# Kernel tuning notes

Measured on AMD Instinct MI355X. Metric: run time of the kernel, lower is better.

The kernel has to match this reference:

```python
import jax, jax.numpy as jnp
import numpy as np

N_NODES = 50000
N_EDGES = 800000
D = 128
BN_EPS = 1e-5


def setup_inputs() -> dict:
    key = jax.random.key(0)
    k1, k2, k3, k4 = jax.random.split(key, 4)
    feature = jax.random.normal(k1, (N_NODES, D), dtype=jnp.float32)
    W = jax.random.normal(k2, (D, D), dtype=jnp.float32) * (1.0 / np.sqrt(D))
    b = jnp.zeros((D,), dtype=jnp.float32)
    gamma = jnp.ones((D,), dtype=jnp.float32)
    beta = jnp.zeros((D,), dtype=jnp.float32)
    src = jax.random.randint(k3, (N_EDGES,), 0, N_NODES, dtype=jnp.int64)
    dst = jax.random.randint(k4, (N_EDGES,), 0, N_NODES, dtype=jnp.int64)
    return {"feature": feature, "W": W, "b": b, "gamma": gamma, "beta": beta,
            "src": src, "dst": dst}


def reference(feature, W, b, gamma, beta, src, dst):
    # --- message passing: copy_u + mean over in-neighbors ---
    n = feature.shape[0]
    msgs = feature[src]  # [E, D] gather of source node features
    agg = jax.ops.segment_sum(msgs, dst, num_segments=n)  # [N, D]
    deg = jax.ops.segment_sum(jnp.ones((src.shape[0],), feature.dtype), dst,
                              num_segments=n)  # [N]
    h = jnp.where(deg[:, None] > 0, agg / jnp.maximum(deg, 1.0)[:, None], 0.0)
    # --- node apply: linear ---
    h = h @ W.T + b
    # --- BatchNorm1d (training mode: biased batch stats over node dim) ---
    mu = jnp.mean(h, axis=0)
    var = jnp.mean(jnp.square(h - mu), axis=0)
    h = (h - mu) / jnp.sqrt(var + BN_EPS) * gamma + beta
    # --- activation + residual (dropout p=0 is identity) ---
    h = jax.nn.relu(h)
    h = feature + h
    return h
```

## Files before the change

kernel.cpp:

```cpp
#include <hip/hip_runtime.h>
#include <cstddef>
#include <cstdint>

#define N_NODES 50000
#define N_EDGES 800000
#define D 128
#define BN_EPS 1e-5f

#define NBUCKET 782
#define BCAP 1536
#define PART_BLOCKS 256
#define PART_CHUNK 3125
#define SLOTS 48
#define SLOTS_P 50
#define GEMM_CHUNKS 1563
#define GEMM_GRID   512
#define FEAT_V8     (N_NODES * D / 8)
#define SLICE_V8    (N_NODES * 4)
#define W_V8        (D * D / 8)
#define CAST_BLOCKS ((FEAT_V8 + W_V8 + 255) / 256)
#define ZERO_V4     3192

typedef __attribute__((ext_vector_type(8))) short short8_t;
typedef __attribute__((ext_vector_type(8))) unsigned short u16x8;
typedef __attribute__((ext_vector_type(4))) float f32x4;
typedef __attribute__((ext_vector_type(4))) int i32x4;

#define WS_STAT_OFF    0
#define WS_GCUR_OFF    1024
#define WS_WB_OFF      51072
#define WS_CLAIM_OFF   83840
#define WS_HB_OFF      4888448
#define WS_H2_OFF      17688448
#define WS_FB_OFF      30488448

static __device__ __forceinline__ unsigned short f2bf(float x) {
    unsigned u = __float_as_uint(x);
    unsigned r = (u + 0x7fffu + ((u >> 16) & 1u)) >> 16;
    return (unsigned short)r;
}
static __device__ __forceinline__ float bf2f(unsigned short v) {
    return __uint_as_float(((unsigned)v) << 16);
}

__global__ __launch_bounds__(256) void prezero_k(i32x4* __restrict__ zws) {
    int i = blockIdx.x * 256 + threadIdx.x;
    if (i < ZERO_V4) zws[i] = (i32x4){0, 0, 0, 0};
}

__global__ __launch_bounds__(256) void castpart_k(const float* __restrict__ feat,
                                                  const float* __restrict__ W,
                                                  u16x8* __restrict__ fb,
                                                  u16x8* __restrict__ wb,
                                                  const int* __restrict__ src,
                                                  const int* __restrict__ dst,
                                                  int* __restrict__ gcur,
                                                  unsigned* __restrict__ claims) {
    __shared__ unsigned pk[PART_CHUNK];
    __shared__ int hist[NBUCKET];
    __shared__ int base_l[NBUCKET];
    const int t = threadIdx.x;

    if (blockIdx.x < PART_BLOCKS) {
        const int base = blockIdx.x * PART_CHUNK;

        for (int b = t; b < NBUCKET; b += 256) hist[b] = 0;
        __syncthreads();

        for (int i = t; i < PART_CHUNK; i += 256) {
            int s = src[base + i];
            int d = dst[base + i];
            pk[i] = ((unsigned)s << 16) | (unsigned)d;
            atomicAdd(&hist[d >> 6], 1);
        }
        __syncthreads();

        for (int b = t; b < NBUCKET; b += 256) {
            int h = hist[b];
            base_l[b] = h ? atomicAdd(gcur + b * 16, h) : 0;
            hist[b] = 0;
        }
        __syncthreads();

        for (int i = t; i < PART_CHUNK; i += 256) {
            unsigned u = pk[i];
            int bkt = (int)(u & 0xffffu) >> 6;
            int k = atomicAdd(&hist[bkt], 1);
            int pos = base_l[bkt] + k;
            if (pos < BCAP) claims[bkt * BCAP + pos] = u;
        }
    } else {
        int i = (blockIdx.x - PART_BLOCKS) * 256 + t;
        if (i < FEAT_V8) {
            int q  = i / SLICE_V8;
            int r  = i - q * SLICE_V8;
            int n  = r >> 2, oc = r & 3;
            const f32x4* fp = reinterpret_cast<const f32x4*>(feat + n * D + q * 32 + oc * 8);
            f32x4 x0 = __builtin_nontemporal_load(fp);
            f32x4 x1 = __builtin_nontemporal_load(fp + 1);
            u16x8 o;
            o[0] = f2bf(x0.x); o[1] = f2bf(x0.y); o[2] = f2bf(x0.z); o[3] = f2bf(x0.w);
            o[4] = f2bf(x1.x); o[5] = f2bf(x1.y); o[6] = f2bf(x1.z); o[7] = f2bf(x1.w);
            __builtin_nontemporal_store(o, fb + i);
        } else if (i < FEAT_V8 + W_V8) {
            int j = i - FEAT_V8;
            const f32x4* fp = reinterpret_cast<const f32x4*>(W) + j * 2;
            f32x4 x0 = __builtin_nontemporal_load(fp);
            f32x4 x1 = __builtin_nontemporal_load(fp + 1);
            u16x8 o;
            o[0] = f2bf(x0.x); o[1] = f2bf(x0.y); o[2] = f2bf(x0.z); o[3] = f2bf(x0.w);
            o[4] = f2bf(x1.x); o[5] = f2bf(x1.y); o[6] = f2bf(x1.z); o[7] = f2bf(x1.w);
            __builtin_nontemporal_store(o, wb + j);
        }
    }
}

__global__ __launch_bounds__(256) void bingather_k(const int* __restrict__ gcur,
                                                   const unsigned* __restrict__ claims,
                                                   const u16x8* __restrict__ fb,
                                                   u16x8* __restrict__ hb) {
    __shared__ unsigned short ebl[64 * SLOTS_P];
    __shared__ int lcnt[64];
    const int t = threadIdx.x;
    const int b = blockIdx.x >> 2;
    const int q = blockIdx.x & 3;
    const u16x8* fbq = fb + (size_t)q * SLICE_V8;

    if (t < 64) lcnt[t] = 0;
    __syncthreads();

    const int n = min(gcur[b * 16], BCAP);
    const unsigned* cp = claims + b * BCAP;
    for (int i = t; i < n; i += 256) {
        unsigned u = cp[i];
        int dl = (int)(u & 63u);
        int k = atomicAdd(&lcnt[dl], 1);
        if (k < SLOTS) ebl[dl * SLOTS_P + k] = (unsigned short)(u >> 16);
    }
    __syncthreads();

    const int nl = t >> 2;
    const int oc = t & 3;
    const int node = (b << 6) + nl;
    const int deg = lcnt[nl];
    const int nd  = min(deg, SLOTS);
    const unsigned short* slots = ebl + nl * SLOTS_P;

    float a[8];
#pragma unroll
    for (int i = 0; i < 8; ++i) a[i] = 0.f;

    int e = 0;
    for (; e + 4 <= nd; e += 4) {
        int s0 = slots[e],     s1 = slots[e + 1];
        int s2 = slots[e + 2], s3 = slots[e + 3];
        u16x8 v0 = fbq[s0 * 4 + oc];
        u16x8 v1 = fbq[s1 * 4 + oc];
        u16x8 v2 = fbq[s2 * 4 + oc];
        u16x8 v3 = fbq[s3 * 4 + oc];
#pragma unroll
        for (int i = 0; i < 8; ++i) a[i] += (bf2f(v0[i]) + bf2f(v1[i])) +
                                            (bf2f(v2[i]) + bf2f(v3[i]));
    }
    for (; e < nd; ++e) {
        u16x8 v0 = fbq[(int)slots[e] * 4 + oc];
#pragma unroll
        for (int i = 0; i < 8; ++i) a[i] += bf2f(v0[i]);
    }

    if (node < N_NODES) {
        float inv = (deg > 0) ? 1.f / (float)deg : 0.f;
        u16x8 o;
#pragma unroll
        for (int i = 0; i < 8; ++i) o[i] = f2bf(a[i] * inv);
        hb[(size_t)q * SLICE_V8 + node * 4 + oc] = o;
    }
}

__global__ __launch_bounds__(256) void gemm_mfma_k(const u16x8* __restrict__ hb,
                                                   const u16x8* __restrict__ wb,
                                                   const float* __restrict__ bias,
                                                   unsigned short* __restrict__ h2,
                                                   float* __restrict__ colsum,
                                                   float* __restrict__ colsumsq) {
    const int wave = threadIdx.x >> 6;
    const int lane = threadIdx.x & 63;
    const int wm = wave >> 1, wn = wave & 1;
    const int l15 = lane & 15, l4 = lane >> 4;

    short8_t bf[4][4];
#pragma unroll
    for (int t = 0; t < 4; ++t) {
        const int col = wn * 64 + t * 16 + l15;
#pragma unroll
        for (int s = 0; s < 4; ++s) {
            u16x8 w = wb[col * 16 + s * 4 + l4];
            short8_t b8;
#pragma unroll
            for (int i = 0; i < 8; ++i) b8[i] = (short)w[i];
            bf[t][s] = b8;
        }
    }
    float bc[4];
#pragma unroll
    for (int t = 0; t < 4; ++t) bc[t] = bias[wn * 64 + t * 16 + l15];

    float s1[4] = {0.f, 0.f, 0.f, 0.f};
    float s2[4] = {0.f, 0.f, 0.f, 0.f};

    for (int chunk = blockIdx.x; chunk < GEMM_CHUNKS; chunk += gridDim.x) {
        const int rbase = chunk * 32 + wm * 16;
        const int arow = min(rbase + l15, N_NODES - 1);
        short8_t af[4];
#pragma unroll
        for (int s = 0; s < 4; ++s) {
            u16x8 hv8 = hb[(size_t)s * SLICE_V8 + arow * 4 + l4];
            short8_t t8;
#pragma unroll
            for (int i = 0; i < 8; ++i) t8[i] = (short)hv8[i];
            af[s] = t8;
        }

        f32x4 acc[4];
#pragma unroll
        for (int t = 0; t < 4; ++t) acc[t] = (f32x4){0.f, 0.f, 0.f, 0.f};

#pragma unroll
        for (int s = 0; s < 4; ++s)
#pragma unroll
            for (int t = 0; t < 4; ++t)
                acc[t] = __builtin_amdgcn_mfma_f32_16x16x32_bf16(af[s], bf[t][s],
                                                                 acc[t], 0, 0, 0);

        const int orow0 = rbase + l4 * 4;
#pragma unroll
        for (int t = 0; t < 4; ++t) {
            const int col = wn * 64 + t * 16 + l15;
#pragma unroll
            for (int r = 0; r < 4; ++r) {
                const int row = orow0 + r;
                if (row < N_NODES) {
                    float hv = acc[t][r] + bc[t];
                    h2[(size_t)row * D + col] = f2bf(hv);
                    s1[t] += hv;
                    s2[t] += hv * hv;
                }
            }
        }
    }

#pragma unroll
    for (int t = 0; t < 4; ++t) {
        s1[t] += __shfl_xor(s1[t], 16); s1[t] += __shfl_xor(s1[t], 32);
        s2[t] += __shfl_xor(s2[t], 16); s2[t] += __shfl_xor(s2[t], 32);
    }
    if (lane < 16) {
#pragma unroll
        for (int t = 0; t < 4; ++t) {
            int col = wn * 64 + t * 16 + lane;
            atomicAdd(colsum + col, s1[t]);
            atomicAdd(colsumsq + col, s2[t]);
        }
    }
}

__global__ __launch_bounds__(256) void epilogue_k(const u16x8* __restrict__ h2v,
                                                  const float* __restrict__ feat,
                                                  const float* __restrict__ colsum,
                                                  const float* __restrict__ colsumsq,
                                                  const float* __restrict__ gamma,
                                                  const float* __restrict__ beta,
                                                  float* __restrict__ out) {
    int idx = blockIdx.x * 256 + threadIdx.x;
    if (idx >= FEAT_V8) return;
    const int colb = (idx * 8) & 127;
    const float inv_n = 1.0f / N_NODES;

    u16x8 hv8 = h2v[idx];
    const float4* fp = reinterpret_cast<const float4*>(feat) + idx * 2;
    float4 fv0 = fp[0], fv1 = fp[1];
    float4 o0, o1;
#pragma unroll
    for (int i = 0; i < 8; ++i) {
        int c = colb + i;
        float mu  = colsum[c] * inv_n;
        float var = colsumsq[c] * inv_n - mu * mu;
        float a   = gamma[c] * rsqrtf(var + BN_EPS);
        float bb  = beta[c] - mu * a;
        float hv  = bf2f(hv8[i]);
        float fv  = (i < 4) ? (&fv0.x)[i] : (&fv1.x)[i - 4];
        float ov  = fv + fmaxf(hv * a + bb, 0.f);
        if (i < 4) (&o0.x)[i] = ov; else (&o1.x)[i - 4] = ov;
    }
    float4* op = reinterpret_cast<float4*>(out) + idx * 2;
    op[0] = o0;
    op[1] = o1;
}

extern "C" void kernel_launch(void* const* d_in, const int* in_sizes, int n_in,
                              void* d_out, int out_size, void* d_ws, size_t ws_size,
                              hipStream_t stream) {
    const float* feature = (const float*)d_in[0];
    const float* W       = (const float*)d_in[1];
    const float* b       = (const float*)d_in[2];
    const float* gamma   = (const float*)d_in[3];
    const float* beta    = (const float*)d_in[4];
    const int*   src     = (const int*)d_in[5];
    const int*   dst     = (const int*)d_in[6];
    float* out = (float*)d_out;

    char* ws = (char*)d_ws;
    float*          colsum   = (float*)(ws + WS_STAT_OFF);
    float*          colsumsq = colsum + 128;
    int*            gcur     = (int*)(ws + WS_GCUR_OFF);
    u16x8*          wb       = (u16x8*)(ws + WS_WB_OFF);
    unsigned*       claims   = (unsigned*)(ws + WS_CLAIM_OFF);
    u16x8*          hb       = (u16x8*)(ws + WS_HB_OFF);
    unsigned short* h2       = (unsigned short*)(ws + WS_H2_OFF);
    u16x8*          fb       = (u16x8*)(ws + WS_FB_OFF);

    prezero_k<<<13, 256, 0, stream>>>((i32x4*)ws);
    castpart_k<<<PART_BLOCKS + CAST_BLOCKS, 256, 0, stream>>>(
        feature, W, fb, wb, src, dst, gcur, claims);
    bingather_k<<<NBUCKET * 4, 256, 0, stream>>>(gcur, claims, fb, hb);
    gemm_mfma_k<<<GEMM_GRID, 256, 0, stream>>>(hb, wb, b, h2, colsum, colsumsq);
    epilogue_k<<<(FEAT_V8 + 255) / 256, 256, 0, stream>>>(
        (u16x8*)h2, feature, colsum, colsumsq, gamma, beta, out);
}
```

Baseline: 105.3 us.

## Fuse GEMM and BatchNorm epilogue into one cooperative kernel with grid sync

The GEMM kernel and the BatchNorm/ReLU/residual epilogue kernel become a single cooperative launch, with a grid-wide barrier after the column-statistics atomics. Each thread computes its per-column scale and shift once, then loops over row chunks writing the output. This removes one kernel launch and the per-element recomputation of the column statistics. It adds grid-sync overhead and requires all 512 blocks to be co-resident. The src/dst index loads also switch to nontemporal loads.

```diff
diff --git a/kernel.cpp b/kernel.cpp
--- a/kernel.cpp
+++ b/kernel.cpp
@@ -1,6 +1,9 @@
 #include <hip/hip_runtime.h>
+#include <hip/hip_cooperative_groups.h>
 #include <cstddef>
 #include <cstdint>
+
+namespace cg = cooperative_groups;
 
 #define N_NODES 50000
 #define N_EDGES 800000
@@ -68,8 +71,8 @@
         __syncthreads();
 
         for (int i = t; i < PART_CHUNK; i += 256) {
-            int s = src[base + i];
-            int d = dst[base + i];
+            int s = __builtin_nontemporal_load(src + base + i);
+            int d = __builtin_nontemporal_load(dst + base + i);
             pk[i] = ((unsigned)s << 16) | (unsigned)d;
             atomicAdd(&hist[d >> 6], 1);
         }
@@ -177,12 +180,16 @@
     }
 }
 
-__global__ __launch_bounds__(256) void gemm_mfma_k(const u16x8* __restrict__ hb,
-                                                   const u16x8* __restrict__ wb,
-                                                   const float* __restrict__ bias,
-                                                   unsigned short* __restrict__ h2,
-                                                   float* __restrict__ colsum,
-                                                   float* __restrict__ colsumsq) {
+__global__ __launch_bounds__(256) void gemmepi_k(const u16x8* __restrict__ hb,
+                                                 const u16x8* __restrict__ wb,
+                                                 const float* __restrict__ bias,
+                                                 unsigned short* __restrict__ h2,
+                                                 float* __restrict__ colsum,
+                                                 float* __restrict__ colsumsq,
+                                                 const float* __restrict__ gamma,
+                                                 const float* __restrict__ beta,
+                                                 const float* __restrict__ feat,
+                                                 float* __restrict__ out) {
     const int wave = threadIdx.x >> 6;
     const int lane = threadIdx.x & 63;
     const int wm = wave >> 1, wn = wave & 1;
@@ -262,39 +269,48 @@
             atomicAdd(colsumsq + col, s2[t]);
         }
     }
-}
-
-__global__ __launch_bounds__(256) void epilogue_k(const u16x8* __restrict__ h2v,
-                                                  const float* __restrict__ feat,
-                                                  const float* __restrict__ colsum,
-                                                  const float* __restrict__ colsumsq,
-                                                  const float* __restrict__ gamma,
-                                                  const float* __restrict__ beta,
-                                                  float* __restrict__ out) {
-    int idx = blockIdx.x * 256 + threadIdx.x;
-    if (idx >= FEAT_V8) return;
-    const int colb = (idx * 8) & 127;
+
+    cg::this_grid().sync();
+
     const float inv_n = 1.0f / N_NODES;
-
-    u16x8 hv8 = h2v[idx];
-    const float4* fp = reinterpret_cast<const float4*>(feat) + idx * 2;
-    float4 fv0 = fp[0], fv1 = fp[1];
-    float4 o0, o1;
+    const int colb = (threadIdx.x & 15) * 8;
+    float av[8], bv[8];
 #pragma unroll
     for (int i = 0; i < 8; ++i) {
         int c = colb + i;
         float mu  = colsum[c] * inv_n;
         float var = colsumsq[c] * inv_n - mu * mu;
         float a   = gamma[c] * rsqrtf(var + BN_EPS);
-        float bb  = beta[c] - mu * a;
-        float hv  = bf2f(hv8[i]);
-        float fv  = (i < 4) ? (&fv0.x)[i] : (&fv1.x)[i - 4];
-        float ov  = fv + fmaxf(hv * a + bb, 0.f);
-        if (i < 4) (&o0.x)[i] = ov; else (&o1.x)[i - 4] = ov;
-    }
-    float4* op = reinterpret_cast<float4*>(out) + idx * 2;
-    op[0] = o0;
-    op[1] = o1;
+        av[i] = a;
+        bv[i] = beta[c] - mu * a;
+    }
+    const u16x8* h2v = reinterpret_cast<const u16x8*>(h2);
+
+    for (int chunk = blockIdx.x; chunk < GEMM_CHUNKS; chunk += gridDim.x) {
+        const int rbase = chunk * 32;
+#pragma unroll
+        for (int rep = 0; rep < 2; ++rep) {
+            int j = rep * 256 + threadIdx.x;
+            int row = rbase + (j >> 4);
+            if (row < N_NODES) {
+                int idx = row * 16 + (j & 15);
+                u16x8 hv8 = h2v[idx];
+                const float4* fp = reinterpret_cast<const float4*>(feat) + idx * 2;
+                float4 fv0 = fp[0], fv1 = fp[1];
+                float4 o0, o1;
+#pragma unroll
+                for (int i = 0; i < 8; ++i) {
+                    float hv = bf2f(hv8[i]);
+                    float fv = (i < 4) ? (&fv0.x)[i] : (&fv1.x)[i - 4];
+                    float ov = fv + fmaxf(hv * av[i] + bv[i], 0.f);
+                    if (i < 4) (&o0.x)[i] = ov; else (&o1.x)[i - 4] = ov;
+                }
+                float4* op = reinterpret_cast<float4*>(out) + idx * 2;
+                op[0] = o0;
+                op[1] = o1;
+            }
+        }
+    }
 }
 
 extern "C" void kernel_launch(void* const* d_in, const int* in_sizes, int n_in,
@@ -323,7 +339,20 @@
     castpart_k<<<PART_BLOCKS + CAST_BLOCKS, 256, 0, stream>>>(
         feature, W, fb, wb, src, dst, gcur, claims);
     bingather_k<<<NBUCKET * 4, 256, 0, stream>>>(gcur, claims, fb, hb);
-    gemm_mfma_k<<<GEMM_GRID, 256, 0, stream>>>(hb, wb, b, h2, colsum, colsumsq);
-    epilogue_k<<<(FEAT_V8 + 255) / 256, 256, 0, stream>>>(
-        (u16x8*)h2, feature, colsum, colsumsq, gamma, beta, out);
-}
+
+    const u16x8*          hb_p   = hb;
+    const u16x8*          wb_p   = wb;
+    const float*          b_p    = b;
+    unsigned short*       h2_p   = h2;
+    float*                cs_p   = colsum;
+    float*                cq_p   = colsumsq;
+    const float*          g_p    = gamma;
+    const float*          bt_p   = beta;
+    const float*          f_p    = feature;
+    float*                out_p  = out;
+    void* kargs[] = {(void*)&hb_p, (void*)&wb_p, (void*)&b_p, (void*)&h2_p,
+                     (void*)&cs_p, (void*)&cq_p, (void*)&g_p, (void*)&bt_p,
+                     (void*)&f_p, (void*)&out_p};
+    hipLaunchCooperativeKernel((void*)gemmepi_k, dim3(GEMM_GRID), dim3(256),
+                               kargs, 0, stream);
+}
```

Measured after the change: 142.4 us. +35.2%, slower.
